# Performance work log

Hardware: AMD Instinct MI355X
Metric: run time of the kernel (lower is better)

Reference implementation:

```python
import jax, jax.numpy as jnp
import numpy as np

NUM_EMBEDDINGS = 1024
EMBEDDING_DIM = 256
COMMITMENT_COST = 0.25


def setup_inputs() -> dict:
    key = jax.random.key(0)
    k1, k2 = jax.random.split(key)
    latents = jax.random.normal(k1, (64, EMBEDDING_DIM, 32, 32), dtype=jnp.float32)
    # embedding init: uniform(-1/K, 1/K)
    scale = 1.0 / NUM_EMBEDDINGS
    embedding = jax.random.uniform(k2, (NUM_EMBEDDINGS, EMBEDDING_DIM),
                                   dtype=jnp.float32, minval=-scale, maxval=scale)
    return {"latents": latents, "embedding": embedding}


def reference(latents, embedding):
    B, C, H, W = latents.shape  # C == EMBEDDING_DIM
    lat_t = jnp.transpose(latents, (0, 2, 3, 1))           # [B,H,W,D]
    flat = lat_t.reshape(-1, C)                             # [N,D]
    distances = (jnp.sum(flat * flat, axis=1, keepdims=True)
                 + jnp.sum(embedding * embedding, axis=1)
                 - 2.0 * jnp.matmul(flat, embedding.T))    # [N,K]
    indices = jnp.argmin(distances, axis=1)                 # [N]
    # gather replaces the one-hot matmul (same math)
    quant_flat = embedding[indices]                         # [N,D]
    quant = quant_flat.reshape(lat_t.shape)                 # [B,H,W,D]
    quant = jnp.transpose(quant, (0, 3, 1, 2))              # [B,C,H,W]
    e_latent_loss = jnp.mean((jax.lax.stop_gradient(quant) - latents) ** 2)
    q_latent_loss = jnp.mean((quant - jax.lax.stop_gradient(latents)) ** 2)
    loss = q_latent_loss + COMMITMENT_COST * e_latent_loss
    # straight-through estimator
    quant_st = latents + jax.lax.stop_gradient(quant - latents)
    return quant_st, loss, indices.reshape(B, H, W)
```

## Files before the change

### kernel.cpp

```cpp
#include <hip/hip_runtime.h>
#include <math.h>


#define DIM 256
#define BSTRIDE 262144
#define OUT_LOSS 16777216
#define OUT_IDX  16777217
#define MARGIN_S 3e-4f

#define RG 8
#define RTILE 32
#define RSTRIDE 260

#define WS_LOSS  0
#define WS_COUNT 8
#define WS_ENORM 64
#define WS_EMBH  8192
#define WS_SEL   532480
#define WS_WL    794624

typedef __attribute__((ext_vector_type(8))) short short8;
typedef __attribute__((ext_vector_type(4))) float f32x4;

__device__ inline unsigned short f2bf(float f) {
  unsigned u = __float_as_uint(f);
  unsigned r = 0x7FFFu + ((u >> 16) & 1u);
  return (unsigned short)((u + r) >> 16);
}
__device__ inline float bf2f(unsigned short h) {
  return __uint_as_float(((unsigned)h) << 16);
}

__global__ void k_prep(const float* __restrict__ emb, float* __restrict__ enormQ,
                       double* __restrict__ lossAcc, int* __restrict__ count) {
  const int k = blockIdx.x * 64 + threadIdx.x;
  if (blockIdx.x == 0 && threadIdx.x == 0) { *lossAcc = 0.0; *count = 0; }
  if (k >= 1024) return;
  const float* e = emb + (size_t)k * DIM;
  float blk[2];
  #pragma unroll
  for (int h = 0; h < 2; ++h) {
    const float* a = e + h * 128;
    float r[8];
    #pragma unroll
    for (int j = 0; j < 8; ++j) r[j] = __fmul_rn(a[j], a[j]);
    for (int i = 8; i < 128; i += 8)
      #pragma unroll
      for (int j = 0; j < 8; ++j) r[j] = __fadd_rn(r[j], __fmul_rn(a[i+j], a[i+j]));
    blk[h] = __fadd_rn(__fadd_rn(__fadd_rn(r[0], r[1]), __fadd_rn(r[2], r[3])),
                       __fadd_rn(__fadd_rn(r[4], r[5]), __fadd_rn(r[6], r[7])));
  }
  enormQ[k] = __fadd_rn(blk[0], blk[1]);
}

__global__ void k_embconv(const float* __restrict__ emb, unsigned short* __restrict__ embHi) {
  const int i = (blockIdx.x * 256 + threadIdx.x) * 4;
  float4 v = *(const float4*)(emb + i);
  unsigned r0 = (unsigned)f2bf(v.x) | ((unsigned)f2bf(v.y) << 16);
  unsigned r1 = (unsigned)f2bf(v.z) | ((unsigned)f2bf(v.w) << 16);
  uint2 st; st.x = r0; st.y = r1;
  *(uint2*)(embHi + i) = st;
}

__launch_bounds__(256, 2)
__global__ void k_score(const float* __restrict__ lat,
                        const unsigned short* __restrict__ embHi,
                        const float* __restrict__ enormQ,
                        int* __restrict__ selIdx, float* __restrict__ out,
                        int* __restrict__ count, int* __restrict__ worklist) {
  __shared__ __align__(16) unsigned short sB[2 * 16 * 264];
  __shared__ float sNorm[1024];

  const int t = threadIdx.x;
  const int w = t >> 6;
  const int L = t & 63;
  const int lane15 = L & 15;
  const int quad = L >> 4;

  const int pix0 = blockIdx.x * 64;
  const int bImg = pix0 >> 10;
  const int hw0 = pix0 & 1023;

  for (int i = t; i < 1024; i += 256) sNorm[i] = enormQ[i];

  const int myPixHw = hw0 + w * 16 + lane15;
  const float* latPix = lat + (size_t)bImg * BSTRIDE + myPixHw;
  short8 aHi[8], aLo[8];
  #pragma unroll
  for (int ks = 0; ks < 8; ++ks) {
    #pragma unroll
    for (int j = 0; j < 8; ++j) {
      float f = latPix[(size_t)(ks * 32 + quad * 8 + j) * 1024];
      unsigned short hb = f2bf(f);
      unsigned short lb = f2bf(f - bf2f(hb));
      aHi[ks][j] = (short)hb;
      aLo[ks][j] = (short)lb;
    }
  }

  float b1[4], b2[4];
  int i1[4], i2[4];
  #pragma unroll
  for (int r = 0; r < 4; ++r) { b1[r] = INFINITY; b2[r] = INFINITY; i1[r] = 0x7fffffff; i2[r] = 0x7fffffff; }

  const int s0 = t, s1 = 256 + t;
  const int n0 = s0 >> 5, o0 = s0 & 31;
  const int n1 = s1 >> 5, o1 = s1 & 31;

  {
    short8 p0 = *(const short8*)(embHi + ((size_t)(0 * 16 + n0) * 256 + o0 * 8));
    short8 p1 = *(const short8*)(embHi + ((size_t)(0 * 16 + n1) * 256 + o1 * 8));
    *(short8*)(sB + n0 * 264 + o0 * 8) = p0;
    *(short8*)(sB + n1 * 264 + o1 * 8) = p1;
  }
  __syncthreads();

  for (int ch = 0; ch < 64; ++ch) {
    const int cur = ch & 1;
    short8 p0, p1;
    if (ch < 63) {
      p0 = *(const short8*)(embHi + ((size_t)((ch + 1) * 16 + n0) * 256 + o0 * 8));
      p1 = *(const short8*)(embHi + ((size_t)((ch + 1) * 16 + n1) * 256 + o1 * 8));
    }
    f32x4 acc = {0.f, 0.f, 0.f, 0.f};
    const unsigned short* bbuf = sB + cur * (16 * 264);
    #pragma unroll
    for (int ks = 0; ks < 8; ++ks) {
      short8 bfrag = *(const short8*)(bbuf + lane15 * 264 + ks * 32 + quad * 8);
      acc = __builtin_amdgcn_mfma_f32_16x16x32_bf16(aHi[ks], bfrag, acc, 0, 0, 0);
      acc = __builtin_amdgcn_mfma_f32_16x16x32_bf16(aLo[ks], bfrag, acc, 0, 0, 0);
    }
    const int n = ch * 16 + lane15;
    const float en = sNorm[n];
    #pragma unroll
    for (int r = 0; r < 4; ++r) {
      float s = fmaf(-2.0f, acc[r], en);
      if (s < b1[r])      { b2[r] = b1[r]; i2[r] = i1[r]; b1[r] = s; i1[r] = n; }
      else if (s < b2[r]) { b2[r] = s; i2[r] = n; }
    }
    if (ch < 63) {
      __syncthreads();
      unsigned short* nb = sB + (1 - cur) * (16 * 264);
      *(short8*)(nb + n0 * 264 + o0 * 8) = p0;
      *(short8*)(nb + n1 * 264 + o1 * 8) = p1;
      __syncthreads();
    }
  }

  #pragma unroll
  for (int m = 1; m <= 8; m <<= 1) {
    #pragma unroll
    for (int r = 0; r < 4; ++r) {
      float ob1 = __shfl_xor(b1[r], m), ob2 = __shfl_xor(b2[r], m);
      int oi1 = __shfl_xor(i1[r], m), oi2 = __shfl_xor(i2[r], m);
      bool aF = (b1[r] < ob1) || (b1[r] == ob1 && i1[r] < oi1);
      float w1 = aF ? b1[r] : ob1;  int wi1 = aF ? i1[r] : oi1;
      float lf = aF ? ob1 : b1[r];  int lfi = aF ? oi1 : i1[r];
      float ws = aF ? b2[r] : ob2;  int wsi = aF ? i2[r] : oi2;
      bool sF = (ws < lf) || (ws == lf && wsi < lfi);
      b1[r] = w1; i1[r] = wi1;
      b2[r] = sF ? ws : lf; i2[r] = sF ? wsi : lfi;
    }
  }
  if (lane15 == 0) {
    #pragma unroll
    for (int r = 0; r < 4; ++r) {
      const int pix = pix0 + w * 16 + quad * 4 + r;
      if (b2[r] - b1[r] >= MARGIN_S) {
        selIdx[pix] = i1[r];
        out[OUT_IDX + pix] = (float)i1[r];
      } else {
        int pos = atomicAdd(count, 1);
        worklist[pos] = pix;
      }
    }
  }
}

__launch_bounds__(256, 2)
__global__ void k_refine(const float* __restrict__ lat, const float* __restrict__ emb,
                         const float* __restrict__ enormQ,
                         const int* __restrict__ count, const int* __restrict__ worklist,
                         int* __restrict__ selIdx, float* __restrict__ out) {
  __shared__ __align__(16) float sE[RTILE * RSTRIDE];
  __shared__ __align__(16) float sX[RG * RSTRIDE];
  __shared__ float sSx[RG];
  const int t = threadIdx.x;
  const int cnt = *count;
  if (cnt == 0) return;
  const int ngroups = (cnt + RG - 1) / RG;
  const int w = t >> 6, lane = t & 63;
  const int sub = lane >> 5;
  const int kLane = lane & 31;
  const int pixSlot = w * 2 + sub;

  for (int g = blockIdx.x; g < ngroups; g += gridDim.x) {
    {
      const int p = t >> 5, c0 = t & 31;
      int wi = g * RG + p; if (wi >= cnt) wi = cnt - 1;
      const int pix = worklist[wi];
      const float* latB = lat + (size_t)(pix >> 10) * BSTRIDE + (pix & 1023);
      #pragma unroll
      for (int i = 0; i < 8; ++i) {
        int c = c0 + 32 * i;
        sX[p * RSTRIDE + c] = latB[(size_t)c * 1024];
      }
    }
    __syncthreads();
    if (t < RG) {
      const float* a0 = sX + t * RSTRIDE;
      float blk[2];
      #pragma unroll
      for (int h = 0; h < 2; ++h) {
        const float* a = a0 + h * 128;
        float r[8];
        #pragma unroll
        for (int j = 0; j < 8; ++j) r[j] = __fmul_rn(a[j], a[j]);
        for (int i = 8; i < 128; i += 8)
          #pragma unroll
          for (int j = 0; j < 8; ++j) r[j] = __fadd_rn(r[j], __fmul_rn(a[i+j], a[i+j]));
        blk[h] = __fadd_rn(__fadd_rn(__fadd_rn(r[0], r[1]), __fadd_rn(r[2], r[3])),
                           __fadd_rn(__fadd_rn(r[4], r[5]), __fadd_rn(r[6], r[7])));
      }
      sSx[t] = __fadd_rn(blk[0], blk[1]);
    }

    float best = INFINITY; int bi = 0x7fffffff;
    const float* xrow = sX + pixSlot * RSTRIDE;
    for (int tile = 0; tile < 32; ++tile) {
      __syncthreads();
      {
        const int r = t >> 3, q0 = t & 7;
        const float* src = emb + (size_t)(tile * RTILE + r) * 256;
        #pragma unroll
        for (int i = 0; i < 8; ++i) {
          int q = q0 + 8 * i;
          *(float4*)(sE + r * RSTRIDE + q * 4) = *(const float4*)(src + q * 4);
        }
      }
      __syncthreads();
      const float* erow = sE + kLane * RSTRIDE;
      float d = 0.f;
      for (int c = 0; c < 256; c += 4) {
        float4 xv = *(const float4*)(xrow + c);
        float4 ev = *(const float4*)(erow + c);
        d = fmaf(xv.x, ev.x, d); d = fmaf(xv.y, ev.y, d);
        d = fmaf(xv.z, ev.z, d); d = fmaf(xv.w, ev.w, d);
      }
      const int k = tile * RTILE + kLane;
      float dq = __fsub_rn(__fadd_rn(sSx[pixSlot], enormQ[k]), __fmul_rn(2.0f, d));
      if (dq < best) { best = dq; bi = k; }
    }
    for (int off = 16; off > 0; off >>= 1) {
      float ob = __shfl_down(best, off);
      int oi = __shfl_down(bi, off);
      if (ob < best || (ob == best && oi < bi)) { best = ob; bi = oi; }
    }
    if (kLane == 0) {
      const int wi = g * RG + pixSlot;
      if (wi < cnt) {
        const int pix = worklist[wi];
        selIdx[pix] = bi;
        out[OUT_IDX + pix] = (float)bi;
      }
    }
    __syncthreads();
  }
}

__global__ void k_gather(const float* __restrict__ lat, const float* __restrict__ emb,
                         const int* __restrict__ selIdx,
                         float* __restrict__ out, double* __restrict__ lossAcc) {
  __shared__ int sIdx[64];
  const int t = threadIdx.x;
  const int pix0 = blockIdx.x * 64;
  const int b = pix0 >> 10;
  const int hw0 = pix0 & 1023;
  const float* latBase = lat + (size_t)b * BSTRIDE + hw0;

  if (t < 64) sIdx[t] = selIdx[pix0 + t];
  __syncthreads();

  const int cSub = t >> 4;
  const int p4 = (t & 15) * 4;
  const int k0 = sIdx[p4], k1 = sIdx[p4+1], k2 = sIdx[p4+2], k3 = sIdx[p4+3];
  double lsum = 0.0;
  #pragma unroll 4
  for (int i = 0; i < 16; ++i) {
    int c = i * 16 + cSub;
    float4 l = *(const float4*)(latBase + (size_t)c * 1024 + p4);
    float q0 = emb[k0 * DIM + c], q1 = emb[k1 * DIM + c],
          q2 = emb[k2 * DIM + c], q3 = emb[k3 * DIM + c];
    float d0 = q0 - l.x, d1 = q1 - l.y, d2 = q2 - l.z, d3 = q3 - l.w;
    float4 o; o.x = l.x + d0; o.y = l.y + d1; o.z = l.z + d2; o.w = l.w + d3;
    *(float4*)(out + (size_t)b * BSTRIDE + (size_t)c * 1024 + hw0 + p4) = o;
    lsum += (double)d0*d0 + (double)d1*d1 + (double)d2*d2 + (double)d3*d3;
  }
  for (int off = 32; off > 0; off >>= 1) lsum += __shfl_down(lsum, off);
  if ((t & 63) == 0) atomicAdd(lossAcc, lsum);
}

__global__ void k_loss(const double* __restrict__ lossAcc, float* __restrict__ out) {
  double m = *lossAcc * (1.0 / 16777216.0);
  out[OUT_LOSS] = (float)(1.25 * m);
}

extern "C" void kernel_launch(void* const* d_in, const int* in_sizes, int n_in,
                              void* d_out, int out_size, void* d_ws, size_t ws_size,
                              hipStream_t stream) {
  const float* lat = (const float*)d_in[0];
  const float* emb = (const float*)d_in[1];
  float* out = (float*)d_out;
  char* ws = (char*)d_ws;
  double* lossAcc = (double*)(ws + WS_LOSS);
  int* count = (int*)(ws + WS_COUNT);
  float* enormQ = (float*)(ws + WS_ENORM);
  unsigned short* embHi = (unsigned short*)(ws + WS_EMBH);
  int* selIdx = (int*)(ws + WS_SEL);
  int* worklist = (int*)(ws + WS_WL);

  k_prep<<<dim3(16), dim3(64), 0, stream>>>(emb, enormQ, lossAcc, count);
  k_embconv<<<dim3(256), dim3(256), 0, stream>>>(emb, embHi);
  k_score<<<dim3(1024), dim3(256), 0, stream>>>(lat, embHi, enormQ, selIdx, out, count, worklist);
  k_refine<<<dim3(1024), dim3(256), 0, stream>>>(lat, emb, enormQ, count, worklist, selIdx, out);
  k_gather<<<dim3(1024), dim3(256), 0, stream>>>(lat, emb, selIdx, out, lossAcc);
  k_loss<<<dim3(1), dim3(1), 0, stream>>>(lossAcc, out);
}
```

Baseline: 388.1 us.

## Enlarge score tile to 2x2 MFMA blocks and stage codebook via direct global-to-LDS loads

The scoring kernel now handles 128 pixels per block, with each wave computing two pixel tiles against 32 codewords per chunk. The A fragments and B fragments are reused across four accumulators. Codebook chunks are copied straight into LDS with global_load_lds in an interleaved layout, which removes the register round trip and one of the two barriers per chunk. The goal is higher MFMA density and less LDS/global traffic per flop. In exchange the kernel holds twice as many A registers, which risks lower occupancy or spills, and the grid halves to 512 blocks.

```diff
diff --git a/kernel.cpp b/kernel.cpp
--- a/kernel.cpp
+++ b/kernel.cpp
@@ -68,7 +68,7 @@
                         const float* __restrict__ enormQ,
                         int* __restrict__ selIdx, float* __restrict__ out,
                         int* __restrict__ count, int* __restrict__ worklist) {
-  __shared__ __align__(16) unsigned short sB[2 * 16 * 264];
+  __shared__ __align__(16) unsigned short sB[2 * 8192];
   __shared__ float sNorm[1024];
 
   const int t = threadIdx.x;
@@ -77,98 +77,127 @@
   const int lane15 = L & 15;
   const int quad = L >> 4;
 
-  const int pix0 = blockIdx.x * 64;
+  const int pix0 = blockIdx.x * 128;
   const int bImg = pix0 >> 10;
   const int hw0 = pix0 & 1023;
 
+  const int nSrc = L & 31;
+  const int oSub = L >> 5;
+
+  #pragma unroll
+  for (int i = 0; i < 4; ++i) {
+    const int o = (w * 4 + i) * 2 + oSub;
+    const unsigned short* src = embHi + ((size_t)nSrc * 256 + o * 8);
+    unsigned short* dst = sB + (w * 4 + i) * 512;
+    __builtin_amdgcn_global_load_lds(
+        (const __attribute__((address_space(1))) unsigned int*)src,
+        (__attribute__((address_space(3))) unsigned int*)dst, 16, 0, 0);
+  }
+
   for (int i = t; i < 1024; i += 256) sNorm[i] = enormQ[i];
 
-  const int myPixHw = hw0 + w * 16 + lane15;
-  const float* latPix = lat + (size_t)bImg * BSTRIDE + myPixHw;
-  short8 aHi[8], aLo[8];
+  const float* latP0 = lat + (size_t)bImg * BSTRIDE + hw0 + w * 32 + lane15;
+  const float* latP1 = latP0 + 16;
+  short8 aHi0[8], aLo0[8], aHi1[8], aLo1[8];
   #pragma unroll
   for (int ks = 0; ks < 8; ++ks) {
     #pragma unroll
     for (int j = 0; j < 8; ++j) {
-      float f = latPix[(size_t)(ks * 32 + quad * 8 + j) * 1024];
-      unsigned short hb = f2bf(f);
-      unsigned short lb = f2bf(f - bf2f(hb));
-      aHi[ks][j] = (short)hb;
-      aLo[ks][j] = (short)lb;
-    }
-  }
-
-  float b1[4], b2[4];
-  int i1[4], i2[4];
-  #pragma unroll
-  for (int r = 0; r < 4; ++r) { b1[r] = INFINITY; b2[r] = INFINITY; i1[r] = 0x7fffffff; i2[r] = 0x7fffffff; }
-
-  const int s0 = t, s1 = 256 + t;
-  const int n0 = s0 >> 5, o0 = s0 & 31;
-  const int n1 = s1 >> 5, o1 = s1 & 31;
-
-  {
-    short8 p0 = *(const short8*)(embHi + ((size_t)(0 * 16 + n0) * 256 + o0 * 8));
-    short8 p1 = *(const short8*)(embHi + ((size_t)(0 * 16 + n1) * 256 + o1 * 8));
-    *(short8*)(sB + n0 * 264 + o0 * 8) = p0;
-    *(short8*)(sB + n1 * 264 + o1 * 8) = p1;
-  }
+      const size_t off = (size_t)(ks * 32 + quad * 8 + j) * 1024;
+      float f0 = latP0[off];
+      float f1 = latP1[off];
+      unsigned short h0 = f2bf(f0);
+      unsigned short h1 = f2bf(f1);
+      aHi0[ks][j] = (short)h0; aLo0[ks][j] = (short)f2bf(f0 - bf2f(h0));
+      aHi1[ks][j] = (short)h1; aLo1[ks][j] = (short)f2bf(f1 - bf2f(h1));
+    }
+  }
+
+  float b1[8], b2[8];
+  int i1[8], i2[8];
+  #pragma unroll
+  for (int p = 0; p < 8; ++p) { b1[p] = INFINITY; b2[p] = INFINITY; i1[p] = 0x7fffffff; i2[p] = 0x7fffffff; }
+
   __syncthreads();
 
-  for (int ch = 0; ch < 64; ++ch) {
+  for (int ch = 0; ch < 32; ++ch) {
     const int cur = ch & 1;
-    short8 p0, p1;
-    if (ch < 63) {
-      p0 = *(const short8*)(embHi + ((size_t)((ch + 1) * 16 + n0) * 256 + o0 * 8));
-      p1 = *(const short8*)(embHi + ((size_t)((ch + 1) * 16 + n1) * 256 + o1 * 8));
-    }
-    f32x4 acc = {0.f, 0.f, 0.f, 0.f};
-    const unsigned short* bbuf = sB + cur * (16 * 264);
+    if (ch < 31) {
+      #pragma unroll
+      for (int i = 0; i < 4; ++i) {
+        const int o = (w * 4 + i) * 2 + oSub;
+        const unsigned short* src = embHi + ((size_t)((ch + 1) * 32 + nSrc) * 256 + o * 8);
+        unsigned short* dst = sB + (1 - cur) * 8192 + (w * 4 + i) * 512;
+        __builtin_amdgcn_global_load_lds(
+            (const __attribute__((address_space(1))) unsigned int*)src,
+            (__attribute__((address_space(3))) unsigned int*)dst, 16, 0, 0);
+      }
+    }
+    const unsigned short* bbuf = sB + cur * 8192;
+    f32x4 acc0a = {0.f,0.f,0.f,0.f}, acc1a = {0.f,0.f,0.f,0.f};
+    f32x4 acc0b = {0.f,0.f,0.f,0.f}, acc1b = {0.f,0.f,0.f,0.f};
     #pragma unroll
     for (int ks = 0; ks < 8; ++ks) {
-      short8 bfrag = *(const short8*)(bbuf + lane15 * 264 + ks * 32 + quad * 8);
-      acc = __builtin_amdgcn_mfma_f32_16x16x32_bf16(aHi[ks], bfrag, acc, 0, 0, 0);
-      acc = __builtin_amdgcn_mfma_f32_16x16x32_bf16(aLo[ks], bfrag, acc, 0, 0, 0);
-    }
-    const int n = ch * 16 + lane15;
-    const float en = sNorm[n];
+      const unsigned short* base = bbuf + (size_t)(ks * 128 + quad * 32) * 8;
+      short8 bf0 = *(const short8*)(base + lane15 * 8);
+      short8 bf1 = *(const short8*)(base + (16 + lane15) * 8);
+      acc0a = __builtin_amdgcn_mfma_f32_16x16x32_bf16(aHi0[ks], bf0, acc0a, 0, 0, 0);
+      acc0a = __builtin_amdgcn_mfma_f32_16x16x32_bf16(aLo0[ks], bf0, acc0a, 0, 0, 0);
+      acc1a = __builtin_amdgcn_mfma_f32_16x16x32_bf16(aHi1[ks], bf0, acc1a, 0, 0, 0);
+      acc1a = __builtin_amdgcn_mfma_f32_16x16x32_bf16(aLo1[ks], bf0, acc1a, 0, 0, 0);
+      acc0b = __builtin_amdgcn_mfma_f32_16x16x32_bf16(aHi0[ks], bf1, acc0b, 0, 0, 0);
+      acc0b = __builtin_amdgcn_mfma_f32_16x16x32_bf16(aLo0[ks], bf1, acc0b, 0, 0, 0);
+      acc1b = __builtin_amdgcn_mfma_f32_16x16x32_bf16(aHi1[ks], bf1, acc1b, 0, 0, 0);
+      acc1b = __builtin_amdgcn_mfma_f32_16x16x32_bf16(aLo1[ks], bf1, acc1b, 0, 0, 0);
+    }
+    const int n0 = ch * 32 + lane15;
+    const float en0 = sNorm[n0];
+    const float en1 = sNorm[n0 + 16];
     #pragma unroll
     for (int r = 0; r < 4; ++r) {
-      float s = fmaf(-2.0f, acc[r], en);
-      if (s < b1[r])      { b2[r] = b1[r]; i2[r] = i1[r]; b1[r] = s; i1[r] = n; }
-      else if (s < b2[r]) { b2[r] = s; i2[r] = n; }
-    }
-    if (ch < 63) {
-      __syncthreads();
-      unsigned short* nb = sB + (1 - cur) * (16 * 264);
-      *(short8*)(nb + n0 * 264 + o0 * 8) = p0;
-      *(short8*)(nb + n1 * 264 + o1 * 8) = p1;
-      __syncthreads();
-    }
+      float s = fmaf(-2.0f, acc0a[r], en0);
+      if (s < b1[r])      { b2[r] = b1[r]; i2[r] = i1[r]; b1[r] = s; i1[r] = n0; }
+      else if (s < b2[r]) { b2[r] = s; i2[r] = n0; }
+      s = fmaf(-2.0f, acc1a[r], en0);
+      if (s < b1[4+r])      { b2[4+r] = b1[4+r]; i2[4+r] = i1[4+r]; b1[4+r] = s; i1[4+r] = n0; }
+      else if (s < b2[4+r]) { b2[4+r] = s; i2[4+r] = n0; }
+    }
+    #pragma unroll
+    for (int r = 0; r < 4; ++r) {
+      const int n1 = n0 + 16;
+      float s = fmaf(-2.0f, acc0b[r], en1);
+      if (s < b1[r])      { b2[r] = b1[r]; i2[r] = i1[r]; b1[r] = s; i1[r] = n1; }
+      else if (s < b2[r]) { b2[r] = s; i2[r] = n1; }
+      s = fmaf(-2.0f, acc1b[r], en1);
+      if (s < b1[4+r])      { b2[4+r] = b1[4+r]; i2[4+r] = i1[4+r]; b1[4+r] = s; i1[4+r] = n1; }
+      else if (s < b2[4+r]) { b2[4+r] = s; i2[4+r] = n1; }
+    }
+    if (ch < 31) __syncthreads();
   }
 
   #pragma unroll
   for (int m = 1; m <= 8; m <<= 1) {
     #pragma unroll
-    for (int r = 0; r < 4; ++r) {
-      float ob1 = __shfl_xor(b1[r], m), ob2 = __shfl_xor(b2[r], m);
-      int oi1 = __shfl_xor(i1[r], m), oi2 = __shfl_xor(i2[r], m);
-      bool aF = (b1[r] < ob1) || (b1[r] == ob1 && i1[r] < oi1);
-      float w1 = aF ? b1[r] : ob1;  int wi1 = aF ? i1[r] : oi1;
-      float lf = aF ? ob1 : b1[r];  int lfi = aF ? oi1 : i1[r];
-      float ws = aF ? b2[r] : ob2;  int wsi = aF ? i2[r] : oi2;
+    for (int p = 0; p < 8; ++p) {
+      float ob1 = __shfl_xor(b1[p], m), ob2 = __shfl_xor(b2[p], m);
+      int oi1 = __shfl_xor(i1[p], m), oi2 = __shfl_xor(i2[p], m);
+      bool aF = (b1[p] < ob1) || (b1[p] == ob1 && i1[p] < oi1);
+      float w1 = aF ? b1[p] : ob1;  int wi1 = aF ? i1[p] : oi1;
+      float lf = aF ? ob1 : b1[p];  int lfi = aF ? oi1 : i1[p];
+      float ws = aF ? b2[p] : ob2;  int wsi = aF ? i2[p] : oi2;
       bool sF = (ws < lf) || (ws == lf && wsi < lfi);
-      b1[r] = w1; i1[r] = wi1;
-      b2[r] = sF ? ws : lf; i2[r] = sF ? wsi : lfi;
+      b1[p] = w1; i1[p] = wi1;
+      b2[p] = sF ? ws : lf; i2[p] = sF ? wsi : lfi;
     }
   }
   if (lane15 == 0) {
     #pragma unroll
-    for (int r = 0; r < 4; ++r) {
-      const int pix = pix0 + w * 16 + quad * 4 + r;
-      if (b2[r] - b1[r] >= MARGIN_S) {
-        selIdx[pix] = i1[r];
-        out[OUT_IDX + pix] = (float)i1[r];
+    for (int p = 0; p < 8; ++p) {
+      const int tl = p >> 2, r = p & 3;
+      const int pix = pix0 + w * 32 + tl * 16 + quad * 4 + r;
+      if (b2[p] - b1[p] >= MARGIN_S) {
+        selIdx[pix] = i1[p];
+        out[OUT_IDX + pix] = (float)i1[p];
       } else {
         int pos = atomicAdd(count, 1);
         worklist[pos] = pix;
@@ -321,7 +350,7 @@
 
   k_prep<<<dim3(16), dim3(64), 0, stream>>>(emb, enormQ, lossAcc, count);
   k_embconv<<<dim3(256), dim3(256), 0, stream>>>(emb, embHi);
-  k_score<<<dim3(1024), dim3(256), 0, stream>>>(lat, embHi, enormQ, selIdx, out, count, worklist);
+  k_score<<<dim3(512), dim3(256), 0, stream>>>(lat, embHi, enormQ, selIdx, out, count, worklist);
   k_refine<<<dim3(1024), dim3(256), 0, stream>>>(lat, emb, enormQ, count, worklist, selIdx, out);
   k_gather<<<dim3(1024), dim3(256), 0, stream>>>(lat, emb, selIdx, out, lossAcc);
   k_loss<<<dim3(1), dim3(1), 0, stream>>>(lossAcc, out);
```

After: 433.7 us. +11.7%, slower.

## Stage codebook tiles via direct global-to-LDS loads with wider 32-code chunks

Applied to the files above, without the earlier changes.

The scoring kernel now streams bf16 codebook tiles into shared memory with async global_load_lds in a fragment-friendly layout. This replaces register-staged copies and cuts the chunk count in half by processing 32 codes per chunk with two accumulators, so each iteration needs one barrier instead of two. Launch bounds are raised to three blocks per CU, and the two prep kernels are merged into one launch. It risks LDS bank conflicts from the new layout, relies on implicit vmcnt waits before the barrier for correctness, and may spill registers under the tighter occupancy target.

```diff
diff --git a/kernel.cpp b/kernel.cpp
--- a/kernel.cpp
+++ b/kernel.cpp
@@ -31,44 +31,44 @@
   return __uint_as_float(((unsigned)h) << 16);
 }
 
-__global__ void k_prep(const float* __restrict__ emb, float* __restrict__ enormQ,
-                       double* __restrict__ lossAcc, int* __restrict__ count) {
-  const int k = blockIdx.x * 64 + threadIdx.x;
-  if (blockIdx.x == 0 && threadIdx.x == 0) { *lossAcc = 0.0; *count = 0; }
-  if (k >= 1024) return;
-  const float* e = emb + (size_t)k * DIM;
-  float blk[2];
-  #pragma unroll
-  for (int h = 0; h < 2; ++h) {
-    const float* a = e + h * 128;
-    float r[8];
-    #pragma unroll
-    for (int j = 0; j < 8; ++j) r[j] = __fmul_rn(a[j], a[j]);
-    for (int i = 8; i < 128; i += 8)
-      #pragma unroll
-      for (int j = 0; j < 8; ++j) r[j] = __fadd_rn(r[j], __fmul_rn(a[i+j], a[i+j]));
-    blk[h] = __fadd_rn(__fadd_rn(__fadd_rn(r[0], r[1]), __fadd_rn(r[2], r[3])),
-                       __fadd_rn(__fadd_rn(r[4], r[5]), __fadd_rn(r[6], r[7])));
-  }
-  enormQ[k] = __fadd_rn(blk[0], blk[1]);
-}
-
-__global__ void k_embconv(const float* __restrict__ emb, unsigned short* __restrict__ embHi) {
-  const int i = (blockIdx.x * 256 + threadIdx.x) * 4;
+__global__ void k_init(const float* __restrict__ emb, unsigned short* __restrict__ embHi,
+                       float* __restrict__ enormQ, double* __restrict__ lossAcc,
+                       int* __restrict__ count) {
+  const int t = threadIdx.x;
+  if (blockIdx.x == 0 && t == 0) { *lossAcc = 0.0; *count = 0; }
+  const int i = (blockIdx.x * 256 + t) * 4;
   float4 v = *(const float4*)(emb + i);
   unsigned r0 = (unsigned)f2bf(v.x) | ((unsigned)f2bf(v.y) << 16);
   unsigned r1 = (unsigned)f2bf(v.z) | ((unsigned)f2bf(v.w) << 16);
   uint2 st; st.x = r0; st.y = r1;
   *(uint2*)(embHi + i) = st;
-}
-
-__launch_bounds__(256, 2)
+  if (blockIdx.x < 4) {
+    const int k = blockIdx.x * 256 + t;
+    const float* e = emb + (size_t)k * DIM;
+    float blk[2];
+    #pragma unroll
+    for (int h = 0; h < 2; ++h) {
+      const float* a = e + h * 128;
+      float r[8];
+      #pragma unroll
+      for (int j = 0; j < 8; ++j) r[j] = __fmul_rn(a[j], a[j]);
+      for (int ii = 8; ii < 128; ii += 8)
+        #pragma unroll
+        for (int j = 0; j < 8; ++j) r[j] = __fadd_rn(r[j], __fmul_rn(a[ii+j], a[ii+j]));
+      blk[h] = __fadd_rn(__fadd_rn(__fadd_rn(r[0], r[1]), __fadd_rn(r[2], r[3])),
+                         __fadd_rn(__fadd_rn(r[4], r[5]), __fadd_rn(r[6], r[7])));
+    }
+    enormQ[k] = __fadd_rn(blk[0], blk[1]);
+  }
+}
+
+__launch_bounds__(256, 3)
 __global__ void k_score(const float* __restrict__ lat,
                         const unsigned short* __restrict__ embHi,
                         const float* __restrict__ enormQ,
                         int* __restrict__ selIdx, float* __restrict__ out,
                         int* __restrict__ count, int* __restrict__ worklist) {
-  __shared__ __align__(16) unsigned short sB[2 * 16 * 264];
+  __shared__ __align__(16) unsigned short sB[2 * 8192];
   __shared__ float sNorm[1024];
 
   const int t = threadIdx.x;
@@ -80,6 +80,19 @@
   const int pix0 = blockIdx.x * 64;
   const int bImg = pix0 >> 10;
   const int hw0 = pix0 & 1023;
+
+  const int nSrc = L & 31;
+  const int oSub = L >> 5;
+
+  #pragma unroll
+  for (int i = 0; i < 4; ++i) {
+    const int o = (w * 4 + i) * 2 + oSub;
+    const unsigned short* src = embHi + ((size_t)nSrc * 256 + o * 8);
+    unsigned short* dst = sB + (w * 4 + i) * 512;
+    __builtin_amdgcn_global_load_lds(
+        (const __attribute__((address_space(1))) unsigned int*)src,
+        (__attribute__((address_space(3))) unsigned int*)dst, 16, 0, 0);
+  }
 
   for (int i = t; i < 1024; i += 256) sNorm[i] = enormQ[i];
 
@@ -103,48 +116,47 @@
   #pragma unroll
   for (int r = 0; r < 4; ++r) { b1[r] = INFINITY; b2[r] = INFINITY; i1[r] = 0x7fffffff; i2[r] = 0x7fffffff; }
 
-  const int s0 = t, s1 = 256 + t;
-  const int n0 = s0 >> 5, o0 = s0 & 31;
-  const int n1 = s1 >> 5, o1 = s1 & 31;
-
-  {
-    short8 p0 = *(const short8*)(embHi + ((size_t)(0 * 16 + n0) * 256 + o0 * 8));
-    short8 p1 = *(const short8*)(embHi + ((size_t)(0 * 16 + n1) * 256 + o1 * 8));
-    *(short8*)(sB + n0 * 264 + o0 * 8) = p0;
-    *(short8*)(sB + n1 * 264 + o1 * 8) = p1;
-  }
   __syncthreads();
 
-  for (int ch = 0; ch < 64; ++ch) {
+  for (int ch = 0; ch < 32; ++ch) {
     const int cur = ch & 1;
-    short8 p0, p1;
-    if (ch < 63) {
-      p0 = *(const short8*)(embHi + ((size_t)((ch + 1) * 16 + n0) * 256 + o0 * 8));
-      p1 = *(const short8*)(embHi + ((size_t)((ch + 1) * 16 + n1) * 256 + o1 * 8));
-    }
-    f32x4 acc = {0.f, 0.f, 0.f, 0.f};
-    const unsigned short* bbuf = sB + cur * (16 * 264);
+    if (ch < 31) {
+      #pragma unroll
+      for (int i = 0; i < 4; ++i) {
+        const int o = (w * 4 + i) * 2 + oSub;
+        const unsigned short* src = embHi + ((size_t)((ch + 1) * 32 + nSrc) * 256 + o * 8);
+        unsigned short* dst = sB + (1 - cur) * 8192 + (w * 4 + i) * 512;
+        __builtin_amdgcn_global_load_lds(
+            (const __attribute__((address_space(1))) unsigned int*)src,
+            (__attribute__((address_space(3))) unsigned int*)dst, 16, 0, 0);
+      }
+    }
+    const unsigned short* bbuf = sB + cur * 8192;
+    f32x4 acc0 = {0.f,0.f,0.f,0.f};
+    f32x4 acc1 = {0.f,0.f,0.f,0.f};
     #pragma unroll
     for (int ks = 0; ks < 8; ++ks) {
-      short8 bfrag = *(const short8*)(bbuf + lane15 * 264 + ks * 32 + quad * 8);
-      acc = __builtin_amdgcn_mfma_f32_16x16x32_bf16(aHi[ks], bfrag, acc, 0, 0, 0);
-      acc = __builtin_amdgcn_mfma_f32_16x16x32_bf16(aLo[ks], bfrag, acc, 0, 0, 0);
-    }
-    const int n = ch * 16 + lane15;
-    const float en = sNorm[n];
+      const unsigned short* base = bbuf + (size_t)(ks * 128 + quad * 32) * 8;
+      short8 bf0 = *(const short8*)(base + lane15 * 8);
+      short8 bf1 = *(const short8*)(base + (16 + lane15) * 8);
+      acc0 = __builtin_amdgcn_mfma_f32_16x16x32_bf16(aHi[ks], bf0, acc0, 0, 0, 0);
+      acc1 = __builtin_amdgcn_mfma_f32_16x16x32_bf16(aHi[ks], bf1, acc1, 0, 0, 0);
+      acc0 = __builtin_amdgcn_mfma_f32_16x16x32_bf16(aLo[ks], bf0, acc0, 0, 0, 0);
+      acc1 = __builtin_amdgcn_mfma_f32_16x16x32_bf16(aLo[ks], bf1, acc1, 0, 0, 0);
+    }
+    const int n0 = ch * 32 + lane15;
+    const float en0 = sNorm[n0];
+    const float en1 = sNorm[n0 + 16];
     #pragma unroll
     for (int r = 0; r < 4; ++r) {
-      float s = fmaf(-2.0f, acc[r], en);
-      if (s < b1[r])      { b2[r] = b1[r]; i2[r] = i1[r]; b1[r] = s; i1[r] = n; }
-      else if (s < b2[r]) { b2[r] = s; i2[r] = n; }
-    }
-    if (ch < 63) {
-      __syncthreads();
-      unsigned short* nb = sB + (1 - cur) * (16 * 264);
-      *(short8*)(nb + n0 * 264 + o0 * 8) = p0;
-      *(short8*)(nb + n1 * 264 + o1 * 8) = p1;
-      __syncthreads();
-    }
+      float s = fmaf(-2.0f, acc0[r], en0);
+      if (s < b1[r])      { b2[r] = b1[r]; i2[r] = i1[r]; b1[r] = s; i1[r] = n0; }
+      else if (s < b2[r]) { b2[r] = s; i2[r] = n0; }
+      float s1 = fmaf(-2.0f, acc1[r], en1);
+      if (s1 < b1[r])      { b2[r] = b1[r]; i2[r] = i1[r]; b1[r] = s1; i1[r] = n0 + 16; }
+      else if (s1 < b2[r]) { b2[r] = s1; i2[r] = n0 + 16; }
+    }
+    if (ch < 31) __syncthreads();
   }
 
   #pragma unroll
@@ -319,8 +331,7 @@
   int* selIdx = (int*)(ws + WS_SEL);
   int* worklist = (int*)(ws + WS_WL);
 
-  k_prep<<<dim3(16), dim3(64), 0, stream>>>(emb, enormQ, lossAcc, count);
-  k_embconv<<<dim3(256), dim3(256), 0, stream>>>(emb, embHi);
+  k_init<<<dim3(256), dim3(256), 0, stream>>>(emb, embHi, enormQ, lossAcc, count);
   k_score<<<dim3(1024), dim3(256), 0, stream>>>(lat, embHi, enormQ, selIdx, out, count, worklist);
   k_refine<<<dim3(1024), dim3(256), 0, stream>>>(lat, emb, enormQ, count, worklist, selIdx, out);
   k_gather<<<dim3(1024), dim3(256), 0, stream>>>(lat, emb, selIdx, out, lossAcc);
```

Measured after the change: 441.1 us. 13.6% more time.
